# Performance work log

Measured on AMD Instinct MI355X. Metric: run time of the kernel, lower is better.

## Reference

```python
import jax, jax.numpy as jnp
import numpy as np

B, S, D, H = 256, 64, 1024, 16
DH = D // H          # 64
BOARD = 8
NREL = 2 * (BOARD - 1) + 1  # 15


def _rel_indices():
    # Relative row/col offsets between all pairs of board squares, shifted to [0, 2*(BOARD-1)]
    coords = np.arange(S)
    row = coords // BOARD
    col = coords % BOARD
    rr = row[:, None] - row[None, :] + (BOARD - 1)  # (S, S)
    rc = col[:, None] - col[None, :] + (BOARD - 1)  # (S, S)
    return jnp.asarray(rr), jnp.asarray(rc)


def setup_inputs() -> dict:
    key = jax.random.key(0)
    ks = jax.random.split(key, 12)
    p = lambda k, sh: jax.random.normal(k, sh, jnp.float32) * 0.02
    return {
        "x": jax.random.normal(ks[0], (B, S, D), jnp.float32),
        "wq": p(ks[1], (D, D)),
        "wk": p(ks[2], (D, D)),
        "wv": p(ks[3], (D, D)),
        "wo": p(ks[4], (D, D)),
        "bo": jnp.zeros((D,), jnp.float32),
        "eq_h": p(ks[5], (NREL, DH)),
        "eq_w": p(ks[6], (NREL, DH)),
        "ek_h": p(ks[7], (NREL, DH)),
        "ek_w": p(ks[8], (NREL, DH)),
        "ev_h": p(ks[9], (NREL, DH)),
        "ev_w": p(ks[10], (NREL, DH)),
    }


def reference(x, wq, wk, wv, wo, bo, eq_h, eq_w, ek_h, ek_w, ev_h, ev_w):
    rr, rc = _rel_indices()
    rel_q = eq_h[rr] + eq_w[rc]  # (S, S, DH)
    rel_k = ek_h[rr] + ek_w[rc]
    rel_v = ev_h[rr] + ev_w[rc]

    def heads(y):
        return y.reshape(B, S, H, DH).transpose(0, 2, 1, 3)  # (B, H, S, DH)

    q = heads(x @ wq.T)
    k = heads(x @ wk.T)
    v = heads(x @ wv.T)

    # (q_i + rq_ij) . (k_j + rk_ij), expanded to avoid the (B,H,S,S,DH) intermediates
    scores = (
        jnp.einsum('bhid,bhjd->bhij', q, k)
        + jnp.einsum('bhid,ijd->bhij', q, rel_k)
        + jnp.einsum('ijd,bhjd->bhij', rel_q, k)
        + jnp.sum(rel_q * rel_k, axis=-1)[None, None]
    )
    attn = jax.nn.softmax(scores / jnp.sqrt(jnp.float32(DH)), axis=-1)  # (B, H, S, S)

    # sum_j attn_ij * (v_j + rv_ij)
    ctx = (
        jnp.einsum('bhij,bhjd->bhid', attn, v)
        + jnp.einsum('bhij,ijd->bhid', attn, rel_v)
    )
    ctx = ctx.transpose(0, 2, 1, 3).reshape(B, S, D)
    return ctx @ wo.T + bo
```

## Files before the change

### kernel.cpp

```cpp
#include <hip/hip_runtime.h>
#include <hip/hip_bf16.h>

typedef __hip_bfloat16 bf16;
typedef __attribute__((ext_vector_type(8))) short short8;
typedef __attribute__((ext_vector_type(8))) unsigned short ushort8;
typedef __attribute__((ext_vector_type(4))) float floatx4;

__device__ __forceinline__ short f2s(float x) {
  bf16 h = __float2bfloat16(x);
  short s;
  __builtin_memcpy(&s, &h, 2);
  return s;
}

__device__ __forceinline__ void gl_lds16(const bf16* g, bf16* l) {
  __builtin_amdgcn_global_load_lds(
      (const __attribute__((address_space(1))) unsigned int*)g,
      (__attribute__((address_space(3))) unsigned int*)l, 16, 0, 0);
}

#define MFMA16(a, b, c) __builtin_amdgcn_mfma_f32_16x16x32_bf16((a), (b), (c), 0, 0, 0)

__device__ __forceinline__ void bar() {
  asm volatile("" ::: "memory");
  __builtin_amdgcn_s_barrier();
  asm volatile("" ::: "memory");
}

#define VMCNT(N) asm volatile("s_waitcnt vmcnt(" #N ")" ::: "memory")

__global__ __launch_bounds__(256) void convert_f32_bf16(
    const float* __restrict__ src, bf16* __restrict__ dst, int n) {
  const int i = (blockIdx.x * 256 + threadIdx.x) * 8;
  if (i + 7 < n) {
    float4 a = *(const float4*)(src + i);
    float4 b = *(const float4*)(src + i + 4);
    short8 r;
    r[0] = f2s(a.x); r[1] = f2s(a.y); r[2] = f2s(a.z); r[3] = f2s(a.w);
    r[4] = f2s(b.x); r[5] = f2s(b.y); r[6] = f2s(b.z); r[7] = f2s(b.w);
    *(short8*)(dst + i) = r;
  }
}

__global__ __launch_bounds__(256) void precompute_tables(
    const float* __restrict__ eqh, const float* __restrict__ eqw,
    const float* __restrict__ ekh, const float* __restrict__ ekw,
    const float* __restrict__ evh, const float* __restrict__ evw,
    bf16* __restrict__ ews, float* __restrict__ S4f)
{
  const int t = threadIdx.x;
  if (t < 96) {
    const int tb = t >> 4, row = t & 15;
    const float* src[6] = {eqh, eqw, ekh, ekw, evh, evw};
    bf16* dst = ews + tb * 1024 + row * 64;
    if (row < 15) {
      const float* s = src[tb] + row * 64;
      #pragma unroll
      for (int d = 0; d < 64; d += 8) {
        float4 a = *(const float4*)(s + d);
        float4 b2 = *(const float4*)(s + d + 4);
        short8 rr;
        rr[0] = f2s(a.x); rr[1] = f2s(a.y); rr[2] = f2s(a.z); rr[3] = f2s(a.w);
        rr[4] = f2s(b2.x); rr[5] = f2s(b2.y); rr[6] = f2s(b2.z); rr[7] = f2s(b2.w);
        *(short8*)(dst + d) = rr;
      }
    } else {
      const short8 z = {0, 0, 0, 0, 0, 0, 0, 0};
      #pragma unroll
      for (int d = 0; d < 64; d += 8) *(short8*)(dst + d) = z;
    }
  }
  if (t < 225) {
    const int r = t / 15, c = t % 15;
    float s = 0.f;
    for (int d = 0; d < 64; ++d)
      s += (eqh[r * 64 + d] + eqw[c * 64 + d]) * (ekh[r * 64 + d] + ekw[c * 64 + d]);
    S4f[t] = s;
  }
}

template <int TAG>
__global__ __launch_bounds__(512, 2) void gemm256(
    const bf16* __restrict__ A,
    const bf16* __restrict__ W0, const bf16* __restrict__ W1, const bf16* __restrict__ W2,
    const float* __restrict__ bias, int hasBias,
    bf16* __restrict__ O0, bf16* __restrict__ O1, bf16* __restrict__ O2,
    float* __restrict__ Ofp, int outF32)
{
  __shared__ bf16 lds[65536];

  const int nx = gridDim.x;
  const int orig = blockIdx.y * nx + blockIdx.x;
  const int xcd = orig & 7;
  const int c = orig >> 3;
  const int bxp = nx >> 3;
  const int bx = xcd * bxp + (c % bxp);
  const int by = c / bxp;

  const int m0 = bx * 256;
  const int which = by >> 2;
  const bf16* W = (which == 0) ? W0 : (which == 1) ? W1 : W2;
  bf16* O = (which == 0) ? O0 : (which == 1) ? O1 : O2;
  const int n0 = (by & 3) * 256;

  const int t = threadIdx.x;
  const int lane = t & 63, w = t >> 6;
  const int wm = w >> 2, wn = w & 3;
  const int quad = lane >> 4, n16 = lane & 15;

  const int srow = (t >> 6) * 16 + ((t & 63) >> 2);
  const int scol = ((t & 3) * 8) ^ (((t >> 5) & 1) << 4);
  const bf16* Abase = A + (m0 + srow) * 1024 + scol;
  const bf16* Bbase = W + (n0 + srow) * 1024 + scol;
  const int wdst = w * 512;

  const int swzq = (quad * 8) ^ ((n16 >> 3) << 4);
  const int aoff = wm * 4096 + n16 * 32 + swzq;
  const int boff = wn * 2048 + n16 * 32 + swzq;

  floatx4 acc[8][4];
  const floatx4 zero4 = {0.f, 0.f, 0.f, 0.f};
  #pragma unroll
  for (int mi = 0; mi < 8; ++mi)
    #pragma unroll
    for (int ni = 0; ni < 4; ++ni) acc[mi][ni] = zero4;

  #pragma unroll
  for (int p = 0; p < 3; ++p) {
    const bf16* ga = Abase + p * 32;
    bf16* la = lds + p * 16384 + wdst;
    gl_lds16(ga, la); gl_lds16(ga + 131072, la + 4096);
    const bf16* gb = Bbase + p * 32;
    bf16* lb = lds + p * 16384 + 8192 + wdst;
    gl_lds16(gb, lb); gl_lds16(gb + 131072, lb + 4096);
  }
  VMCNT(8);
  bar();

#define TILE_STEP(TT, DOSTAGE, WAITSEQ) do {                                   \
    const bf16* bA_ = lds + ((TT) & 3) * 16384;                                \
    const bf16* bB_ = bA_ + 8192;                                              \
    short8 af_[4], bq_[4];                                                     \
    _Pragma("unroll")                                                          \
    for (int mi = 0; mi < 4; ++mi)                                             \
      af_[mi] = *(const short8*)(bA_ + aoff + mi * 512);                       \
    _Pragma("unroll")                                                          \
    for (int ni = 0; ni < 4; ++ni)                                             \
      bq_[ni] = *(const short8*)(bB_ + boff + ni * 512);                       \
    if (DOSTAGE) {                                                             \
      const bf16* g_ = Abase + ((TT) + 3) * 32;                                \
      bf16* l_ = lds + (((TT) + 3) & 3) * 16384 + wdst;                        \
      gl_lds16(g_, l_); gl_lds16(g_ + 131072, l_ + 4096);                      \
    }                                                                          \
    bar();                                                                     \
    __builtin_amdgcn_s_setprio(1);                                             \
    _Pragma("unroll")                                                          \
    for (int mi = 0; mi < 4; ++mi)                                             \
      _Pragma("unroll")                                                        \
      for (int ni = 0; ni < 4; ++ni)                                           \
        acc[mi][ni] = MFMA16(af_[mi], bq_[ni], acc[mi][ni]);                   \
    __builtin_amdgcn_s_setprio(0);                                             \
    _Pragma("unroll")                                                          \
    for (int mi = 0; mi < 4; ++mi)                                             \
      af_[mi] = *(const short8*)(bA_ + aoff + 2048 + mi * 512);                \
    if (DOSTAGE) {                                                             \
      const bf16* g_ = Bbase + ((TT) + 3) * 32;                                \
      bf16* l_ = lds + (((TT) + 3) & 3) * 16384 + 8192 + wdst;                 \
      gl_lds16(g_, l_); gl_lds16(g_ + 131072, l_ + 4096);                      \
    }                                                                          \
    __builtin_amdgcn_s_setprio(1);                                             \
    _Pragma("unroll")                                                          \
    for (int mi = 0; mi < 4; ++mi)                                             \
      _Pragma("unroll")                                                        \
      for (int ni = 0; ni < 4; ++ni)                                           \
        acc[mi + 4][ni] = MFMA16(af_[mi], bq_[ni], acc[mi + 4][ni]);           \
    __builtin_amdgcn_s_setprio(0);                                             \
    WAITSEQ;                                                                   \
  } while (0)

  #pragma unroll 1
  for (int tt = 0; tt < 29; ++tt) {
    TILE_STEP(tt, 1, VMCNT(8); bar());
  }
  TILE_STEP(29, 0, VMCNT(4); bar());
  TILE_STEP(30, 0, VMCNT(0); bar());
  TILE_STEP(31, 0, (void)0);
#undef TILE_STEP

  #pragma unroll
  for (int ni = 0; ni < 4; ++ni) {
    const int col = n0 + wn * 64 + ni * 16 + n16;
    const float bv = hasBias ? bias[col] : 0.f;
    #pragma unroll
    for (int mi = 0; mi < 8; ++mi) {
      #pragma unroll
      for (int r = 0; r < 4; ++r) {
        const int row = m0 + wm * 128 + mi * 16 + quad * 4 + r;
        if (outF32) Ofp[row * 1024 + col] = acc[mi][ni][r] + bv;
        else        O[row * 1024 + col] = __float2bfloat16(acc[mi][ni][r] + bv);
      }
    }
  }
}

template <int TAG>
__global__ __launch_bounds__(256) void gemm_bt(
    const bf16* __restrict__ A,
    const void* __restrict__ W0, const void* __restrict__ W1, const void* __restrict__ W2,
    int wBf,
    const float* __restrict__ bias, int hasBias,
    bf16* __restrict__ O0, bf16* __restrict__ O1, bf16* __restrict__ O2,
    float* __restrict__ Ofp, int outF32)
{
  __shared__ bf16 As[128 * 64];
  __shared__ bf16 Bs[128 * 64];

  const int m0 = blockIdx.x * 128;
  const int by = blockIdx.y;
  const int which = by >> 3;
  const void* W = (which == 0) ? W0 : (which == 1) ? W1 : W2;
  bf16* O = (which == 0) ? O0 : (which == 1) ? O1 : O2;
  const int n0 = (by & 7) * 128;

  const int t = threadIdx.x;
  const int lane = t & 63, w = t >> 6;
  const int lrow = lane >> 3, lcol = (lane & 7) * 8;
  const int wm = w >> 1, wn = w & 1;
  const int quad = lane >> 4, n16 = lane & 15;

  const int swzA = ((lrow & 1) << 5) | (((lrow >> 1) & 3) << 3);
  const int gcol = lcol ^ swzA;
  const int swzR = ((n16 & 1) << 5) | (((n16 >> 1) & 3) << 3);

  floatx4 acc[4][4];
  const floatx4 zero4 = {0.f, 0.f, 0.f, 0.f};
  #pragma unroll
  for (int mi = 0; mi < 4; ++mi)
    #pragma unroll
    for (int ni = 0; ni < 4; ++ni) acc[mi][ni] = zero4;

  const int arowb = m0 + w * 32 + lrow;
  const int browb = n0 + w * 32 + lrow;
  bf16* lau = As + w * 2048;
  bf16* lbu = Bs + w * 2048;

  if (wBf) {
    const bf16* Wb = (const bf16*)W;
    for (int k0 = 0; k0 < 1024; k0 += 64) {
      if (k0) __syncthreads();
      const bf16* ga = A + arowb * 1024 + k0 + gcol;
      const bf16* gw = Wb + browb * 1024 + k0 + gcol;
      #pragma unroll
      for (int c = 0; c < 4; ++c) {
        gl_lds16(ga + c * 8192, lau + c * 512);
        gl_lds16(gw + c * 8192, lbu + c * 512);
      }
      __syncthreads();
      #pragma unroll
      for (int ks = 0; ks < 2; ++ks) {
        short8 af[4], bfv[4];
        #pragma unroll
        for (int mi = 0; mi < 4; ++mi)
          af[mi] = *(const short8*)(As + (wm * 64 + mi * 16 + n16) * 64 +
                                    ((ks * 32 + quad * 8) ^ swzR));
        #pragma unroll
        for (int ni = 0; ni < 4; ++ni)
          bfv[ni] = *(const short8*)(Bs + (wn * 64 + ni * 16 + n16) * 64 +
                                     ((ks * 32 + quad * 8) ^ swzR));
        #pragma unroll
        for (int mi = 0; mi < 4; ++mi)
          #pragma unroll
          for (int ni = 0; ni < 4; ++ni)
            acc[mi][ni] = MFMA16(af[mi], bfv[ni], acc[mi][ni]);
      }
    }
  } else {
    const float* Wf = (const float*)W;
    for (int k0 = 0; k0 < 1024; k0 += 64) {
      short8 rb[4];
      #pragma unroll
      for (int c = 0; c < 4; ++c) {
        const float* f = Wf + (browb + c * 8) * 1024 + k0 + gcol;
        float4 a = *(const float4*)f;
        float4 b = *(const float4*)(f + 4);
        short8 r;
        r[0] = f2s(a.x); r[1] = f2s(a.y); r[2] = f2s(a.z); r[3] = f2s(a.w);
        r[4] = f2s(b.x); r[5] = f2s(b.y); r[6] = f2s(b.z); r[7] = f2s(b.w);
        rb[c] = r;
      }
      if (k0) __syncthreads();
      const bf16* ga = A + arowb * 1024 + k0 + gcol;
      #pragma unroll
      for (int c = 0; c < 4; ++c) {
        gl_lds16(ga + c * 8192, lau + c * 512);
        *(short8*)(lbu + lane * 8 + c * 512) = rb[c];
      }
      __syncthreads();
      #pragma unroll
      for (int ks = 0; ks < 2; ++ks) {
        short8 af[4], bfv[4];
        #pragma unroll
        for (int mi = 0; mi < 4; ++mi)
          af[mi] = *(const short8*)(As + (wm * 64 + mi * 16 + n16) * 64 +
                                    ((ks * 32 + quad * 8) ^ swzR));
        #pragma unroll
        for (int ni = 0; ni < 4; ++ni)
          bfv[ni] = *(const short8*)(Bs + (wn * 64 + ni * 16 + n16) * 64 +
                                     ((ks * 32 + quad * 8) ^ swzR));
        #pragma unroll
        for (int mi = 0; mi < 4; ++mi)
          #pragma unroll
          for (int ni = 0; ni < 4; ++ni)
            acc[mi][ni] = MFMA16(af[mi], bfv[ni], acc[mi][ni]);
      }
    }
  }

  #pragma unroll
  for (int ni = 0; ni < 4; ++ni) {
    const int col = n0 + wn * 64 + ni * 16 + n16;
    const float bv = hasBias ? bias[col] : 0.f;
    #pragma unroll
    for (int mi = 0; mi < 4; ++mi) {
      #pragma unroll
      for (int r = 0; r < 4; ++r) {
        const int row = m0 + wm * 64 + mi * 16 + quad * 4 + r;
        if (outF32) Ofp[row * 1024 + col] = acc[mi][ni][r] + bv;
        else        O[row * 1024 + col] = __float2bfloat16(acc[mi][ni][r] + bv);
      }
    }
  }
}

__global__ __launch_bounds__(256, 3) void attn_rel(
    const bf16* __restrict__ Q, const bf16* __restrict__ Km, const bf16* __restrict__ V,
    const bf16* __restrict__ ews, const float* __restrict__ S4f,
    bf16* __restrict__ Ctx)
{
  __shared__ bf16 vT[64][106];
  __shared__ bf16 pa[64][104];
  __shared__ float Ahs[64][16], Aws[64][16];
  __shared__ float Bhs[15][64], Bws[15][64];
  __shared__ float S4s[225];

  const int t = threadIdx.x;
  const int b = blockIdx.x >> 4, h = blockIdx.x & 15;
  const int base = b * 65536 + h * 64;
  const int lane = t & 63, w = t >> 6;
  const int quad = lane >> 4, n16 = lane & 15;

  const bf16* qrow = Q + base + (w * 16 + n16) * 1024 + quad * 8;
  short8 aq0 = *(const short8*)(qrow);
  short8 aq1 = *(const short8*)(qrow + 32);
  short8 bk0[4], bk1[4];
  #pragma unroll
  for (int nj = 0; nj < 4; ++nj) {
    const bf16* krow = Km + base + (nj * 16 + n16) * 1024 + quad * 8;
    bk0[nj] = *(const short8*)(krow);
    bk1[nj] = *(const short8*)(krow + 32);
  }
  short8 ebf[4][2];
  #pragma unroll
  for (int tb = 0; tb < 4; ++tb) {
    const bf16* er = ews + tb * 1024 + n16 * 64 + quad * 8;
    ebf[tb][0] = *(const short8*)(er);
    ebf[tb][1] = *(const short8*)(er + 32);
  }

  {
    const int r = t >> 2, c0 = (t & 3) * 16;
    const bf16* vrow = V + base + r * 1024 + c0;
    int4 v0 = *(const int4*)(vrow);
    int4 v1 = *(const int4*)(vrow + 8);
    const unsigned short* p0 = (const unsigned short*)&v0;
    const unsigned short* p1 = (const unsigned short*)&v1;
    #pragma unroll
    for (int ii = 0; ii < 8; ++ii) {
      *(unsigned short*)&vT[c0 + ii][r] = p0[ii];
      *(unsigned short*)&vT[c0 + 8 + ii][r] = p1[ii];
    }
    if (t < 60) {
      const int r2 = t >> 2, d0 = (t & 3) * 16;
      ushort8 pe0 = *(const ushort8*)(ews + 4096 + r2 * 64 + d0);
      ushort8 pe1 = *(const ushort8*)(ews + 4096 + r2 * 64 + d0 + 8);
      ushort8 pf0 = *(const ushort8*)(ews + 5120 + r2 * 64 + d0);
      ushort8 pf1 = *(const ushort8*)(ews + 5120 + r2 * 64 + d0 + 8);
      #pragma unroll
      for (int ii = 0; ii < 8; ++ii) {
        *(unsigned short*)&vT[d0 + ii][64 + r2] = pe0[ii];
        *(unsigned short*)&vT[d0 + 8 + ii][64 + r2] = pe1[ii];
        *(unsigned short*)&vT[d0 + ii][79 + r2] = pf0[ii];
        *(unsigned short*)&vT[d0 + 8 + ii][79 + r2] = pf1[ii];
      }
    }
    if (t < 64) {
      *(unsigned short*)&vT[t][94] = 0; *(unsigned short*)&vT[t][95] = 0;
      *(unsigned short*)&pa[t][94] = 0; *(unsigned short*)&pa[t][95] = 0;
    }
    if (t < 225) S4s[t] = S4f[t];
  }

  floatx4 cqk[4];
  #pragma unroll
  for (int nj = 0; nj < 4; ++nj) {
    floatx4 c = {0.f, 0.f, 0.f, 0.f};
    c = MFMA16(aq0, bk0[nj], c);
    c = MFMA16(aq1, bk1[nj], c);
    cqk[nj] = c;
  }
  {
    floatx4 cah = {0.f, 0.f, 0.f, 0.f}, caw = cah, cbh = cah, cbw = cah;
    cah = MFMA16(aq0, ebf[2][0], cah); cah = MFMA16(aq1, ebf[2][1], cah);
    caw = MFMA16(aq0, ebf[3][0], caw); caw = MFMA16(aq1, ebf[3][1], caw);
    cbh = MFMA16(bk0[w], ebf[0][0], cbh); cbh = MFMA16(bk1[w], ebf[0][1], cbh);
    cbw = MFMA16(bk0[w], ebf[1][0], cbw); cbw = MFMA16(bk1[w], ebf[1][1], cbw);
    #pragma unroll
    for (int r = 0; r < 4; ++r) {
      const int i = w * 16 + quad * 4 + r;
      Ahs[i][n16] = cah[r];
      Aws[i][n16] = caw[r];
      if (n16 < 15) { Bhs[n16][i] = cbh[r]; Bws[n16][i] = cbw[r]; }
    }
  }
  __syncthreads();

  const int i_base = w * 16 + quad * 4;
  float xv[4][4];
  #pragma unroll
  for (int nj = 0; nj < 4; ++nj) {
    const int j = nj * 16 + n16;
    const int rowj = j >> 3, colj = j & 7;
    #pragma unroll
    for (int r = 0; r < 4; ++r) {
      const int i = i_base + r;
      const int rowi = i >> 3, coli = i & 7;
      const int rr = rowi - rowj + 7, rc = coli - colj + 7;
      xv[r][nj] = (cqk[nj][r] + Ahs[i][rr] + Aws[i][rc] + Bhs[rr][j] + Bws[rc][j]
                   + S4s[rr * 15 + rc]) * 0.125f;
    }
  }
  #pragma unroll
  for (int r = 0; r < 4; ++r) {
    const int i = i_base + r;
    const int rowi = i >> 3, coli = i & 7;
    float mx = fmaxf(fmaxf(xv[r][0], xv[r][1]), fmaxf(xv[r][2], xv[r][3]));
    #pragma unroll
    for (int off = 1; off < 16; off <<= 1) mx = fmaxf(mx, __shfl_xor(mx, off));
    float p[4];
    float sm = 0.f;
    #pragma unroll
    for (int nj = 0; nj < 4; ++nj) { p[nj] = __expf(xv[r][nj] - mx); sm += p[nj]; }
    #pragma unroll
    for (int off = 1; off < 16; off <<= 1) sm += __shfl_xor(sm, off);
    const float inv = 1.0f / sm;
    #pragma unroll
    for (int nj = 0; nj < 4; ++nj) {
      p[nj] *= inv;
      pa[i][nj * 16 + n16] = __float2bfloat16(p[nj]);
    }
    float ph[4];
    #pragma unroll
    for (int nj = 0; nj < 4; ++nj) {
      float v = p[nj];
      v += __shfl_xor(v, 1); v += __shfl_xor(v, 2); v += __shfl_xor(v, 4);
      ph[nj] = v;
    }
    float s4 = p[0] + p[1] + p[2] + p[3];
    float pw = s4 + __shfl_xor(s4, 8);
    if ((n16 & 7) == 0) {
      const int hh = n16 >> 3;
      #pragma unroll
      for (int nj = 0; nj < 4; ++nj) {
        const int g = nj * 2 + hh;
        pa[i][64 + rowi + 7 - g] = __float2bfloat16(ph[nj]);
      }
    } else if (n16 < 8) {
      const int z = n16 - 1;
      pa[i][64 + (z < rowi ? z : z + 8)] = __float2bfloat16(0.f);
    }
    if (n16 < 8) {
      pa[i][79 + coli + 7 - n16] = __float2bfloat16(pw);
    } else {
      const int z = n16 - 8;
      pa[i][79 + (z < coli ? z : z + 8)] = __float2bfloat16(0.f);
    }
  }
  __threadfence_block();

  short8 ap[3];
  #pragma unroll
  for (int ksb = 0; ksb < 3; ++ksb)
    ap[ksb] = *(const short8*)&pa[w * 16 + n16][ksb * 32 + quad * 8];
  #pragma unroll
  for (int nj = 0; nj < 4; ++nj) {
    floatx4 c = {0.f, 0.f, 0.f, 0.f};
    #pragma unroll
    for (int ksb = 0; ksb < 3; ++ksb) {
      short8 bv = *(const short8*)&vT[nj * 16 + n16][ksb * 32 + quad * 8];
      c = MFMA16(ap[ksb], bv, c);
    }
    #pragma unroll
    for (int r = 0; r < 4; ++r) {
      const int i = i_base + r;
      Ctx[base + i * 1024 + nj * 16 + n16] = __float2bfloat16(c[r]);
    }
  }
}

extern "C" void kernel_launch(void* const* d_in, const int* in_sizes, int n_in,
                              void* d_out, int out_size, void* d_ws, size_t ws_size,
                              hipStream_t stream) {
  const float* x   = (const float*)d_in[0];
  const float* wq  = (const float*)d_in[1];
  const float* wk  = (const float*)d_in[2];
  const float* wv  = (const float*)d_in[3];
  const float* wo  = (const float*)d_in[4];
  const float* bo  = (const float*)d_in[5];
  const float* eqh = (const float*)d_in[6];
  const float* eqw = (const float*)d_in[7];
  const float* ekh = (const float*)d_in[8];
  const float* ekw = (const float*)d_in[9];
  const float* evh = (const float*)d_in[10];
  const float* evw = (const float*)d_in[11];
  float* outf = (float*)d_out;

  const size_t hdr = (ws_size - 16384) & ~(size_t)1023;
  bf16* ewsB = (bf16*)((char*)d_ws + hdr);
  float* S4f = (float*)((char*)d_ws + hdr + 12288);
  precompute_tables<<<1, 256, 0, stream>>>(eqh, eqw, ekh, ekw, evh, evw, ewsB, S4f);

  if (ws_size >= (size_t)73 * 1024 * 1024) {
    bf16* qb = (bf16*)d_ws;
    bf16* kb = qb + 16777216;
    bf16* wqb = kb + 16777216;
    bf16* wkb = wqb + 1048576;
    bf16* wvb = wkb + 1048576;
    bf16* wob = wvb + 1048576;
    bf16* xb = (bf16*)d_out;
    bf16* vb = (bf16*)((char*)d_out + 33554432);

    convert_f32_bf16<<<8192, 256, 0, stream>>>(x, xb, 16777216);
    convert_f32_bf16<<<512, 256, 0, stream>>>(wq, wqb, 1048576);
    convert_f32_bf16<<<512, 256, 0, stream>>>(wk, wkb, 1048576);
    convert_f32_bf16<<<512, 256, 0, stream>>>(wv, wvb, 1048576);
    convert_f32_bf16<<<512, 256, 0, stream>>>(wo, wob, 1048576);

    gemm256<0><<<dim3(64, 12), 512, 0, stream>>>(
        xb, wqb, wkb, wvb, nullptr, 0, qb, kb, vb, nullptr, 0);
    attn_rel<<<dim3(4096), 256, 0, stream>>>(qb, kb, vb, ewsB, S4f, qb);
    gemm256<1><<<dim3(64, 4), 512, 0, stream>>>(
        qb, wob, nullptr, nullptr, bo, 1, nullptr, nullptr, nullptr, outf, 1);
  } else {
    bf16* xb0 = (bf16*)((char*)d_out + 16777216);
    bf16* xb1 = (bf16*)((char*)d_out + 50331648);
    bf16* vQ2 = (bf16*)((char*)d_out + 33554432);
    bf16* qb = (bf16*)d_ws;
    bf16* kb = qb + 8388608;
    const int fastW = (ws_size >= (size_t)42 * 1024 * 1024) ? 1 : 0;
    bf16* wqb = kb + 8388608;
    bf16* wkb = wqb + 1048576;
    bf16* wvb = wkb + 1048576;
    bf16* wob = wvb + 1048576;

    convert_f32_bf16<<<4096, 256, 0, stream>>>(x, xb0, 8388608);
    convert_f32_bf16<<<4096, 256, 0, stream>>>(x + 8388608, xb1, 8388608);
    if (fastW) {
      convert_f32_bf16<<<512, 256, 0, stream>>>(wq, wqb, 1048576);
      convert_f32_bf16<<<512, 256, 0, stream>>>(wk, wkb, 1048576);
      convert_f32_bf16<<<512, 256, 0, stream>>>(wv, wvb, 1048576);
      convert_f32_bf16<<<512, 256, 0, stream>>>(wo, wob, 1048576);
    }

    for (int hh = 0; hh < 2; ++hh) {
      const bf16* xh = hh ? xb1 : xb0;
      if (fastW) {
        gemm256<0><<<dim3(32, 12), 512, 0, stream>>>(
            xh, wqb, wkb, wvb, nullptr, 0, qb, kb, vQ2, nullptr, 0);
      } else {
        gemm_bt<0><<<dim3(64, 24), 256, 0, stream>>>(
            xh, (const void*)wq, (const void*)wk, (const void*)wv,
            0, nullptr, 0, qb, kb, vQ2, nullptr, 0);
      }
      attn_rel<<<dim3(2048), 256, 0, stream>>>(qb, kb, vQ2, ewsB, S4f, qb);
      if (fastW) {
        gemm256<1><<<dim3(32, 4), 512, 0, stream>>>(
            qb, wob, nullptr, nullptr, bo, 1, nullptr, nullptr, nullptr,
            outf + (size_t)hh * 8388608, 1);
      } else {
        gemm_bt<1><<<dim3(64, 8), 256, 0, stream>>>(
            qb, (const void*)wo, nullptr, nullptr,
            0, bo, 1, nullptr, nullptr, nullptr,
            outf + (size_t)hh * 8388608, 1);
      }
    }
  }
}
```

Measured before the change: 377.7 us.

## Restructure QKV GEMM mainloop to double-buffered K=64 tiles with quadrant MFMA ordering

Replaces the 4-stage, K=32 LDS pipeline in the projection GEMM with a 2-buffer scheme that loads K=64 per iteration, halving the loop trip count and the number of barriers. Fragments are read per quadrant, and MFMAs are interleaved with the LDS reads of the next quadrant. The trade-off is a shallower prefetch depth: it waits with vmcnt(0) every iteration, so global-load latency may be exposed. It also raises register pressure from holding more fragments.

```diff
diff --git a/kernel.cpp b/kernel.cpp
--- a/kernel.cpp
+++ b/kernel.cpp
@@ -114,9 +114,7 @@
   const bf16* Bbase = W + (n0 + srow) * 1024 + scol;
   const int wdst = w * 512;
 
-  const int swzq = (quad * 8) ^ ((n16 >> 3) << 4);
-  const int aoff = wm * 4096 + n16 * 32 + swzq;
-  const int boff = wn * 2048 + n16 * 32 + swzq;
+  const int roff = n16 * 32 + ((quad * 8) ^ ((n16 >> 3) << 4));
 
   floatx4 acc[8][4];
   const floatx4 zero4 = {0.f, 0.f, 0.f, 0.f};
@@ -125,67 +123,78 @@
     #pragma unroll
     for (int ni = 0; ni < 4; ++ni) acc[mi][ni] = zero4;
 
-  #pragma unroll
-  for (int p = 0; p < 3; ++p) {
-    const bf16* ga = Abase + p * 32;
-    bf16* la = lds + p * 16384 + wdst;
-    gl_lds16(ga, la); gl_lds16(ga + 131072, la + 4096);
-    const bf16* gb = Bbase + p * 32;
-    bf16* lb = lds + p * 16384 + 8192 + wdst;
-    gl_lds16(gb, lb); gl_lds16(gb + 131072, lb + 4096);
-  }
-  VMCNT(8);
-  bar();
-
-#define TILE_STEP(TT, DOSTAGE, WAITSEQ) do {                                   \
-    const bf16* bA_ = lds + ((TT) & 3) * 16384;                                \
-    const bf16* bB_ = bA_ + 8192;                                              \
-    short8 af_[4], bq_[4];                                                     \
+#define STAGE_AB(TT, BB) do {                                                  \
+    const bf16* gA_ = Abase + (TT) * 64;                                       \
+    const bf16* gB_ = Bbase + (TT) * 64;                                       \
+    bf16* lA_ = lds + (BB) * 32768 + wdst;                                     \
+    bf16* lB_ = lA_ + 16384;                                                   \
+    gl_lds16(gA_,               lA_);                                          \
+    gl_lds16(gA_ + 32,          lA_ + 8192);                                   \
+    gl_lds16(gA_ + 131072,      lA_ + 4096);                                   \
+    gl_lds16(gA_ + 131072 + 32, lA_ + 12288);                                  \
+    gl_lds16(gB_,               lB_);                                          \
+    gl_lds16(gB_ + 32,          lB_ + 8192);                                   \
+    gl_lds16(gB_ + 131072,      lB_ + 4096);                                   \
+    gl_lds16(gB_ + 131072 + 32, lB_ + 12288);                                  \
+  } while (0)
+
+#define READ_A(DST, BUFA, AA)                                                  \
     _Pragma("unroll")                                                          \
-    for (int mi = 0; mi < 4; ++mi)                                             \
-      af_[mi] = *(const short8*)(bA_ + aoff + mi * 512);                       \
+    for (int mi = 0; mi < 4; ++mi) {                                           \
+      DST[mi * 2 + 0] = *(const short8*)((BUFA) +                              \
+          (wm * 8 + (AA) * 4 + mi) * 512 + roff);                              \
+      DST[mi * 2 + 1] = *(const short8*)((BUFA) + 8192 +                       \
+          (wm * 8 + (AA) * 4 + mi) * 512 + roff);                              \
+    }
+
+#define READ_B(DST, BUFB, HH)                                                  \
     _Pragma("unroll")                                                          \
-    for (int ni = 0; ni < 4; ++ni)                                             \
-      bq_[ni] = *(const short8*)(bB_ + boff + ni * 512);                       \
-    if (DOSTAGE) {                                                             \
-      const bf16* g_ = Abase + ((TT) + 3) * 32;                                \
-      bf16* l_ = lds + (((TT) + 3) & 3) * 16384 + wdst;                        \
-      gl_lds16(g_, l_); gl_lds16(g_ + 131072, l_ + 4096);                      \
-    }                                                                          \
-    bar();                                                                     \
+    for (int nj = 0; nj < 2; ++nj) {                                           \
+      DST[nj * 2 + 0] = *(const short8*)((BUFB) +                              \
+          (wn * 4 + (HH) * 2 + nj) * 512 + roff);                              \
+      DST[nj * 2 + 1] = *(const short8*)((BUFB) + 8192 +                       \
+          (wn * 4 + (HH) * 2 + nj) * 512 + roff);                              \
+    }
+
+#define MFMA_Q(AARR, BARR, AA, HH)                                             \
     __builtin_amdgcn_s_setprio(1);                                             \
     _Pragma("unroll")                                                          \
     for (int mi = 0; mi < 4; ++mi)                                             \
       _Pragma("unroll")                                                        \
-      for (int ni = 0; ni < 4; ++ni)                                           \
-        acc[mi][ni] = MFMA16(af_[mi], bq_[ni], acc[mi][ni]);                   \
-    __builtin_amdgcn_s_setprio(0);                                             \
-    _Pragma("unroll")                                                          \
-    for (int mi = 0; mi < 4; ++mi)                                             \
-      af_[mi] = *(const short8*)(bA_ + aoff + 2048 + mi * 512);                \
-    if (DOSTAGE) {                                                             \
-      const bf16* g_ = Bbase + ((TT) + 3) * 32;                                \
-      bf16* l_ = lds + (((TT) + 3) & 3) * 16384 + 8192 + wdst;                 \
-      gl_lds16(g_, l_); gl_lds16(g_ + 131072, l_ + 4096);                      \
-    }                                                                          \
-    __builtin_amdgcn_s_setprio(1);                                             \
-    _Pragma("unroll")                                                          \
-    for (int mi = 0; mi < 4; ++mi)                                             \
-      _Pragma("unroll")                                                        \
-      for (int ni = 0; ni < 4; ++ni)                                           \
-        acc[mi + 4][ni] = MFMA16(af_[mi], bq_[ni], acc[mi + 4][ni]);           \
-    __builtin_amdgcn_s_setprio(0);                                             \
-    WAITSEQ;                                                                   \
-  } while (0)
+      for (int nj = 0; nj < 2; ++nj) {                                         \
+        acc[(AA)*4+mi][(HH)*2+nj] =                                            \
+            MFMA16(AARR[mi*2+0], BARR[nj*2+0], acc[(AA)*4+mi][(HH)*2+nj]);     \
+        acc[(AA)*4+mi][(HH)*2+nj] =                                            \
+            MFMA16(AARR[mi*2+1], BARR[nj*2+1], acc[(AA)*4+mi][(HH)*2+nj]);     \
+      }                                                                        \
+    __builtin_amdgcn_s_setprio(0);
+
+  STAGE_AB(0, 0);
+  VMCNT(0);
+  bar();
 
   #pragma unroll 1
-  for (int tt = 0; tt < 29; ++tt) {
-    TILE_STEP(tt, 1, VMCNT(8); bar());
-  }
-  TILE_STEP(29, 0, VMCNT(4); bar());
-  TILE_STEP(30, 0, VMCNT(0); bar());
-  TILE_STEP(31, 0, (void)0);
-#undef TILE_STEP
+  for (int tt = 0; tt < 16; ++tt) {
+    const int cb = tt & 1;
+    const bf16* bufA = lds + cb * 32768;
+    const bf16* bufB = bufA + 16384;
+    if (tt < 15) STAGE_AB(tt + 1, cb ^ 1);
+    short8 Af0[8], Af1[8], Bf0[4], Bf1[4];
+    READ_A(Af0, bufA, 0);
+    READ_B(Bf0, bufB, 0);
+    MFMA_Q(Af0, Bf0, 0, 0);
+    READ_A(Af1, bufA, 1);
+    MFMA_Q(Af1, Bf0, 1, 0);
+    READ_B(Bf1, bufB, 1);
+    MFMA_Q(Af0, Bf1, 0, 1);
+    MFMA_Q(Af1, Bf1, 1, 1);
+    if (tt < 15) VMCNT(0);
+    bar();
+  }
+#undef STAGE_AB
+#undef READ_A
+#undef READ_B
+#undef MFMA_Q
 
   #pragma unroll
   for (int ni = 0; ni < 4; ++ni) {
```

Result: no change. 376.3 us (-0.4%).
